# Performance work log

Measured on AMD Instinct MI355X. Metric: run time of the kernel, lower is better.

The kernel has to match this reference:

```python
import jax, jax.numpy as jnp
import numpy as np

B, T, I, H, O = 64, 512, 128, 1024, 128
ALPHA = 0.2


def setup_inputs() -> dict:
    key = jax.random.key(0)
    ks = jax.random.split(key, 7)
    inv_sqrt_h = 1.0 / np.sqrt(H)
    return {
        "x": jax.random.normal(ks[0], (B, T, I), dtype=jnp.float32),
        "wi": jax.random.normal(ks[1], (I, H), dtype=jnp.float32) / np.sqrt(I),
        "wrec": jax.random.normal(ks[2], (H, H), dtype=jnp.float32) * inv_sqrt_h,
        "wout": jax.random.normal(ks[3], (H, O), dtype=jnp.float32) * inv_sqrt_h,
        "b": jax.random.normal(ks[4], (H, 1), dtype=jnp.float32) * 0.1,
        "g": jax.random.normal(ks[5], (H, 1), dtype=jnp.float32) * 0.5 + 1.0,
        "h0": jax.random.normal(ks[6], (H,), dtype=jnp.float32) * 0.1,
    }


def reference(x, wi, wrec, wout, b, g, h0):
    # Leaky tanh RNN: h_{t+1} = h_t + alpha*(-h_t + (g*r_t) @ wrec^T + x_t @ wi)
    #                 r_t = tanh(h_t + b); out_t = (g*r_t) @ wout
    gv = g[:, 0]  # (H,)
    bv = b[:, 0]  # (H,)
    batch = x.shape[0]

    r0 = jnp.tanh(h0 + bv)                     # (H,)
    out0 = (gv * r0) @ wout                    # (O,) broadcast over batch

    h_init = jnp.broadcast_to(h0, (batch, h0.shape[0]))
    r_init = jnp.broadcast_to(r0, (batch, h0.shape[0]))

    # precompute input projection for all steps used in the loop (steps 0..T-2)
    xs = jnp.swapaxes(x[:, :-1, :], 0, 1)      # (T-1, B, I)

    def step(carry, x_t):
        h, r = carry
        h = h + ALPHA * (-h + (gv * r) @ wrec.T + x_t @ wi)
        r = jnp.tanh(h + bv)
        out = (gv * r) @ wout                  # (B, O)
        return (h, r), out

    _, outs = jax.lax.scan(step, (h_init, r_init), xs)   # (T-1, B, O)
    outs = jnp.swapaxes(outs, 0, 1)                      # (B, T-1, O)
    out0b = jnp.broadcast_to(out0, (batch, 1, wout.shape[1]))
    return jnp.concatenate([out0b, outs], axis=1)        # (B, T, O)
```

## Files before the change

kernel.cpp:

```cpp
#include <hip/hip_runtime.h>

#define H 1024
#define I_DIM 128
#define O_DIM 128
#define T_DIM 512
#define ALPHA 0.2f
#define NWG 64
#define GSZ 16
#define PLANE_U64 2048
#define GRP_U64   (3 * PLANE_U64)

typedef short short8 __attribute__((ext_vector_type(8)));
typedef float f32x4 __attribute__((ext_vector_type(4)));
typedef unsigned long long ull_alias __attribute__((may_alias));

__device__ __forceinline__ unsigned short f2b(float f) {
    union { float f; unsigned u; } x; x.f = f;
    unsigned u = x.u;
    return (unsigned short)((u + 0x7FFFu + ((u >> 16) & 1u)) >> 16);
}
__device__ __forceinline__ float tanh_fast(float x) {
    float e = __expf(2.0f * x);
    return 1.0f - 2.0f * __builtin_amdgcn_rcpf(e + 1.0f);
}
__device__ __forceinline__ short8 ld8f(const float* __restrict__ p) {
    const float4 a = *(const float4*)p;
    const float4 b = *(const float4*)(p + 4);
    short8 r;
    r[0]=(short)f2b(a.x); r[1]=(short)f2b(a.y); r[2]=(short)f2b(a.z); r[3]=(short)f2b(a.w);
    r[4]=(short)f2b(b.x); r[5]=(short)f2b(b.y); r[6]=(short)f2b(b.z); r[7]=(short)f2b(b.w);
    return r;
}
__device__ __forceinline__ short8 pack8(float4 a, float4 b) {
    short8 r;
    r[0]=(short)f2b(a.x); r[1]=(short)f2b(a.y); r[2]=(short)f2b(a.z); r[3]=(short)f2b(a.w);
    r[4]=(short)f2b(b.x); r[5]=(short)f2b(b.y); r[6]=(short)f2b(b.z); r[7]=(short)f2b(b.w);
    return r;
}
__device__ __forceinline__ void bar_lgkm() {
    asm volatile("s_waitcnt lgkmcnt(0)\n\ts_barrier" ::: "memory");
}

__global__ __launch_bounds__(256, 1) void rnn_kernel(
    const float* __restrict__ x, const float* __restrict__ wi,
    const float* __restrict__ wrec, const float* __restrict__ wout,
    const float* __restrict__ bb, const float* __restrict__ gg,
    const float* __restrict__ h0p, float* __restrict__ out,
    unsigned long long* __restrict__ aG)
{
    __shared__ unsigned short abuf[32 * 512];
    __shared__ unsigned short aloc[1024];
    __shared__ float opart[4 * 128];

    const int tid  = threadIdx.x;
    const int w    = tid >> 6, lane = tid & 63;
    const int n    = lane & 15, q = lane >> 4;
    const int grp  = blockIdx.x & 3;
    const int ji   = blockIdx.x >> 2;
    const int j0   = ji * 64;
    const int j    = j0 + w * 16 + n;
    const int b0   = grp * 16;

    short8 wfr[32];
#pragma unroll
    for (int kt = 0; kt < 32; ++kt)
        wfr[kt] = ld8f(&wrec[(size_t)j * H + kt * 32 + q * 8]);

    short8 wifr[4];
#pragma unroll
    for (int kt = 0; kt < 4; ++kt) {
        short8 v;
#pragma unroll
        for (int i = 0; i < 8; ++i)
            v[i] = (short)f2b(wi[(size_t)(kt * 32 + q * 8 + i) * H + j]);
        wifr[kt] = v;
    }
    short8 wofr[8];
#pragma unroll
    for (int kk = 0; kk < 8; ++kk) {
        short8 v;
        const int kb = (w * 8 + kk) * 32 + q * 8;
#pragma unroll
        for (int i = 0; i < 8; ++i)
            v[i] = (n < 8) ? (short)f2b(wout[(size_t)(kb + i) * O_DIM + ji * 8 + n]) : (short)0;
        wofr[kk] = v;
    }

    const float gv = gg[j], bv = bb[j], h00 = h0p[j];
    float hreg[4];
#pragma unroll
    for (int r = 0; r < 4; ++r) hreg[r] = h00;

    const int kl    = w * 16 + n;
    const int off_l = (kl >> 5) * 512 + ((kl & 31) >> 3) * 128 + (kl & 7);
    const int s_sl  = ji * 4 + w;

    unsigned long long* const gB0 = aG + grp * GRP_U64;
    unsigned long long* const gB1 = aG + (4 + grp) * GRP_U64;

    const int pubA = (lane >> 5) * PLANE_U64 + s_sl * 32 + (lane & 31);
    const int pubB = 2 * PLANE_U64 + s_sl * 32 + lane;
    const int oA   = lane & 31;

    const int perm  = (lane >> 5) * 32 + (lane & 15) * 2 + ((lane >> 4) & 1);
    const int cb    = w * 512 + perm;

    auto publish = [&](int t) {
        asm volatile("" ::: "memory");
        const unsigned long long tagv = (unsigned long long)(unsigned)t << 48;
        unsigned long long* gb = (t & 1) ? gB1 : gB0;
        {
            const ull_alias* opq = (const ull_alias*)&aloc[w * 256 + (oA & 1) * 128 + (oA >> 1) * 8];
            const unsigned long long lo = opq[0], hi = opq[1];
            const unsigned long long d0 = lo & 0x0000FFFFFFFFFFFFull;
            const unsigned long long d1 = ((lo >> 48) | (hi << 16)) & 0x0000FFFFFFFFFFFFull;
            __hip_atomic_store(gb + pubA, ((lane < 32) ? d0 : d1) | tagv,
                               __ATOMIC_RELAXED, __HIP_MEMORY_SCOPE_AGENT);
        }
        if (lane < 32) {
            const ull_alias* opq = (const ull_alias*)&aloc[w * 256 + (lane & 1) * 128 + (lane >> 1) * 8];
            const unsigned long long hi = opq[1];
            const unsigned long long d2 = ((hi >> 32) & 0xFFFFFFFFull) | tagv;
            __hip_atomic_store(gb + pubB, d2, __ATOMIC_RELAXED, __HIP_MEMORY_SCOPE_AGENT);
        }
    };

    auto poll_issue = [&](const unsigned long long* gb,
                          unsigned long long* v0, unsigned long long* v1,
                          unsigned long long* v2) {
#pragma unroll
        for (int i = 0; i < 8; ++i) {
            v0[i] = __hip_atomic_load(gb + cb + i * 64,
                                      __ATOMIC_RELAXED, __HIP_MEMORY_SCOPE_AGENT);
            v1[i] = __hip_atomic_load(gb + PLANE_U64 + cb + i * 64,
                                      __ATOMIC_RELAXED, __HIP_MEMORY_SCOPE_AGENT);
            v2[i] = __hip_atomic_load(gb + 2 * PLANE_U64 + cb + i * 64,
                                      __ATOMIC_RELAXED, __HIP_MEMORY_SCOPE_AGENT);
        }
    };

    auto poll_check = [&](int tv, const unsigned long long* gb,
                          unsigned long long* v0, unsigned long long* v1,
                          unsigned long long* v2) {
        const unsigned tt = (unsigned)tv;
        for (;;) {
            unsigned bad = 0;
#pragma unroll
            for (int i = 0; i < 8; ++i)
                bad |= ((unsigned)(v0[i] >> 48) ^ tt) | ((unsigned)(v1[i] >> 48) ^ tt)
                     | ((unsigned)(v2[i] >> 48) ^ tt);
            if (__all(bad == 0)) break;
            __builtin_amdgcn_s_sleep(1);
            poll_issue(gb, v0, v1, v2);
        }
        asm volatile("" ::: "memory");
    };

    auto unpack = [&](const unsigned long long* v0, const unsigned long long* v1,
                      const unsigned long long* v2) {
#pragma unroll
        for (int i = 0; i < 8; ++i) {
            const unsigned long long ca = v0[i], cb_ = v1[i], cc = v2[i];
            const unsigned long long w01 = (ca & 0xFFFFFFFFull)
                | (((ca >> 32) & 0xFFFFull) << 32) | ((cb_ & 0xFFFFull) << 48);
            const unsigned long long w23 = ((cb_ >> 16) & 0xFFFFFFFFull) | (cc << 32);
            ull_alias* d = (ull_alias*)((char*)abuf + w * 8192 + (i * 64 + lane) * 16);
            d[0] = w01; d[1] = w23;
        }
    };

    auto do_out = [&](int t) {
        f32x4 oa = {0.f, 0.f, 0.f, 0.f};
#pragma unroll
        for (int kk = 0; kk < 8; ++kk) {
            short8 af = *(const short8*)&abuf[(w * 8 + kk) * 512 + lane * 8];
            oa = __builtin_amdgcn_mfma_f32_16x16x32_bf16(af, wofr[kk], oa, 0, 0, 0);
        }
        if (n < 8) {
#pragma unroll
            for (int r = 0; r < 4; ++r) opart[w * 128 + (4 * q + r) * 8 + n] = oa[r];
        }
        bar_lgkm();
        if (tid < 128) {
            float s = opart[tid] + opart[128 + tid] + opart[256 + tid] + opart[384 + tid];
            const int m = tid >> 3, c = tid & 7;
            out[((size_t)(b0 + m) * T_DIM + t) * O_DIM + ji * 8 + c] = s;
        }
    };

    {
        unsigned short a0 = f2b(gv * tanh_fast(h00 + bv));
#pragma unroll
        for (int r = 0; r < 4; ++r) aloc[off_l + (4 * q + r) * 8] = a0;
        publish(0);
    }

    short8 xfr[4];
#pragma unroll
    for (int kt = 0; kt < 4; ++kt)
        xfr[kt] = ld8f(&x[(size_t)(b0 + n) * T_DIM * I_DIM + kt * 32 + q * 8]);

    float4 xr[8];
    unsigned long long pv0[8], pv1[8], pv2[8];

    for (int t = 1; t < T_DIM; ++t) {
        const unsigned long long* gbp = ((t - 1) & 1) ? gB1 : gB0;

        poll_issue(gbp, pv0, pv1, pv2);

        if (t < T_DIM - 1) {
            const float* xp = &x[((size_t)(b0 + n) * T_DIM + t) * I_DIM];
#pragma unroll
            for (int kt = 0; kt < 4; ++kt) {
                xr[2 * kt]     = *(const float4*)(xp + kt * 32 + q * 8);
                xr[2 * kt + 1] = *(const float4*)(xp + kt * 32 + q * 8 + 4);
            }
        }

        f32x4 acc0 = {0.f,0.f,0.f,0.f}, acc1 = {0.f,0.f,0.f,0.f};
        acc0 = __builtin_amdgcn_mfma_f32_16x16x32_bf16(xfr[0], wifr[0], acc0, 0,0,0);
        acc1 = __builtin_amdgcn_mfma_f32_16x16x32_bf16(xfr[1], wifr[1], acc1, 0,0,0);
        acc0 = __builtin_amdgcn_mfma_f32_16x16x32_bf16(xfr[2], wifr[2], acc0, 0,0,0);
        acc1 = __builtin_amdgcn_mfma_f32_16x16x32_bf16(xfr[3], wifr[3], acc1, 0,0,0);

        bar_lgkm();
        poll_check(t - 1, gbp, pv0, pv1, pv2);
        unpack(pv0, pv1, pv2);
        bar_lgkm();

#pragma unroll
        for (int kt = 0; kt < 32; kt += 2) {
            short8 a0f = *(const short8*)&abuf[kt * 512 + lane * 8];
            short8 a1f = *(const short8*)&abuf[(kt + 1) * 512 + lane * 8];
            acc0 = __builtin_amdgcn_mfma_f32_16x16x32_bf16(a0f, wfr[kt],     acc0, 0,0,0);
            acc1 = __builtin_amdgcn_mfma_f32_16x16x32_bf16(a1f, wfr[kt + 1], acc1, 0,0,0);
        }

#pragma unroll
        for (int r = 0; r < 4; ++r) {
            float z  = acc0[r] + acc1[r];
            float hv = (1.0f - ALPHA) * hreg[r] + ALPHA * z;
            hreg[r] = hv;
            aloc[off_l + (4 * q + r) * 8] = f2b(gv * tanh_fast(hv + bv));
        }
        publish(t);

        if (t < T_DIM - 1) {
#pragma unroll
            for (int kt = 0; kt < 4; ++kt)
                xfr[kt] = pack8(xr[2 * kt], xr[2 * kt + 1]);
        }
        do_out(t - 1);
    }

    poll_issue(gB1, pv0, pv1, pv2);
    bar_lgkm();
    poll_check(T_DIM - 1, gB1, pv0, pv1, pv2);
    unpack(pv0, pv1, pv2);
    bar_lgkm();
    do_out(T_DIM - 1);
}

extern "C" void kernel_launch(void* const* d_in, const int* in_sizes, int n_in,
                              void* d_out, int out_size, void* d_ws, size_t ws_size,
                              hipStream_t stream) {
    const float* x    = (const float*)d_in[0];
    const float* wi   = (const float*)d_in[1];
    const float* wrec = (const float*)d_in[2];
    const float* wout = (const float*)d_in[3];
    const float* bb   = (const float*)d_in[4];
    const float* gg   = (const float*)d_in[5];
    const float* h0   = (const float*)d_in[6];
    float* outp = (float*)d_out;

    unsigned long long* aG = (unsigned long long*)d_ws;

    hipMemsetAsync(d_ws, 0xFF, (size_t)2 * 4 * GRP_U64 * 8, stream);
    hipLaunchKernelGGL(rnn_kernel, dim3(NWG), dim3(256), 0, stream,
                       x, wi, wrec, wout, bb, gg, h0, outp, aG);
}
```

Before: 1.792 ms.

## Repartition RNN across 8 batch groups with 32 hidden columns per wave

Changes the work split from 4 batch groups of 16 rows to 8 groups of 8 rows. Each wave now owns 32 hidden units (two 16-column MFMA tiles), holding twice as many recurrent-weight fragments in registers. The output projection is folded into the recurrent MFMA loop, and one barrier per step is removed by reordering poll, unpack and output writes. The aim is to shrink per-step cross-workgroup exchange and synchronization latency. The costs are that half of each MFMA's 16 rows carry no useful batch data, and the larger register footprint could spill.

```diff
diff --git a/kernel.cpp b/kernel.cpp
--- a/kernel.cpp
+++ b/kernel.cpp
@@ -6,12 +6,14 @@
 #define T_DIM 512
 #define ALPHA 0.2f
 #define NWG 64
-#define GSZ 16
-#define PLANE_U64 2048
-#define GRP_U64   (3 * PLANE_U64)
+#define PLANE_U64 1024
+#define PAR_U64   3072
+#define GRPA_U64  6144
+#define ARENA_U64 49152
 
 typedef short short8 __attribute__((ext_vector_type(8)));
 typedef float f32x4 __attribute__((ext_vector_type(4)));
+typedef unsigned long long u64;
 typedef unsigned long long ull_alias __attribute__((may_alias));
 
 __device__ __forceinline__ unsigned short f2b(float f) {
@@ -46,35 +48,46 @@
     const float* __restrict__ wrec, const float* __restrict__ wout,
     const float* __restrict__ bb, const float* __restrict__ gg,
     const float* __restrict__ h0p, float* __restrict__ out,
-    unsigned long long* __restrict__ aG)
+    u64* __restrict__ aG)
 {
-    __shared__ unsigned short abuf[32 * 512];
+    __shared__ unsigned short abuf[8192];
     __shared__ unsigned short aloc[1024];
-    __shared__ float opart[4 * 128];
+    __shared__ float opart[512];
 
     const int tid  = threadIdx.x;
     const int w    = tid >> 6, lane = tid & 63;
-    const int n    = lane & 15, q = lane >> 4;
-    const int grp  = blockIdx.x & 3;
-    const int ji   = blockIdx.x >> 2;
-    const int j0   = ji * 64;
-    const int j    = j0 + w * 16 + n;
-    const int b0   = grp * 16;
-
-    short8 wfr[32];
-#pragma unroll
-    for (int kt = 0; kt < 32; ++kt)
-        wfr[kt] = ld8f(&wrec[(size_t)j * H + kt * 32 + q * 8]);
-
-    short8 wifr[4];
-#pragma unroll
-    for (int kt = 0; kt < 4; ++kt) {
-        short8 v;
-#pragma unroll
-        for (int i = 0; i < 8; ++i)
-            v[i] = (short)f2b(wi[(size_t)(kt * 32 + q * 8 + i) * H + j]);
-        wifr[kt] = v;
-    }
+    const int q    = lane >> 4;
+    const int n16  = lane & 15;
+    const int mm8  = lane & 7;
+    const int q2   = (lane >> 4) & 1;
+    const int b3   = (lane >> 3) & 1;
+    const int grp  = (int)blockIdx.x & 7;
+    const int ji   = (int)blockIdx.x >> 3;
+    const int b0   = grp * 8;
+    const int jb   = ji * 128 + w * 32;
+    const int s_sl = ji * 4 + w;
+    const int cbg  = w * 256 + lane;
+
+    u64* const gB = aG + (size_t)grp * GRPA_U64;
+
+    short8 wfr[64];
+#pragma unroll
+    for (int nt = 0; nt < 2; ++nt)
+#pragma unroll
+        for (int kt = 0; kt < 32; ++kt)
+            wfr[nt * 32 + kt] = ld8f(&wrec[(size_t)(jb + nt * 16 + n16) * H + kt * 32 + q * 8]);
+
+    short8 wifr[8];
+#pragma unroll
+    for (int nt = 0; nt < 2; ++nt)
+#pragma unroll
+        for (int kt = 0; kt < 4; ++kt) {
+            short8 v;
+#pragma unroll
+            for (int i = 0; i < 8; ++i)
+                v[i] = (short)f2b(wi[(size_t)(kt * 32 + q * 8 + i) * H + jb + nt * 16 + n16]);
+            wifr[nt * 4 + kt] = v;
+        }
     short8 wofr[8];
 #pragma unroll
     for (int kk = 0; kk < 8; ++kk) {
@@ -82,183 +95,196 @@
         const int kb = (w * 8 + kk) * 32 + q * 8;
 #pragma unroll
         for (int i = 0; i < 8; ++i)
-            v[i] = (n < 8) ? (short)f2b(wout[(size_t)(kb + i) * O_DIM + ji * 8 + n]) : (short)0;
+            v[i] = (short)f2b(wout[(size_t)(kb + i) * O_DIM + ji * 16 + n16]);
         wofr[kk] = v;
     }
 
-    const float gv = gg[j], bv = bb[j], h00 = h0p[j];
-    float hreg[4];
-#pragma unroll
-    for (int r = 0; r < 4; ++r) hreg[r] = h00;
-
-    const int kl    = w * 16 + n;
-    const int off_l = (kl >> 5) * 512 + ((kl & 31) >> 3) * 128 + (kl & 7);
-    const int s_sl  = ji * 4 + w;
-
-    unsigned long long* const gB0 = aG + grp * GRP_U64;
-    unsigned long long* const gB1 = aG + (4 + grp) * GRP_U64;
-
-    const int pubA = (lane >> 5) * PLANE_U64 + s_sl * 32 + (lane & 31);
-    const int pubB = 2 * PLANE_U64 + s_sl * 32 + lane;
-    const int oA   = lane & 31;
-
-    const int perm  = (lane >> 5) * 32 + (lane & 15) * 2 + ((lane >> 4) & 1);
-    const int cb    = w * 512 + perm;
-
-    auto publish = [&](int t) {
-        asm volatile("" ::: "memory");
-        const unsigned long long tagv = (unsigned long long)(unsigned)t << 48;
-        unsigned long long* gb = (t & 1) ? gB1 : gB0;
-        {
-            const ull_alias* opq = (const ull_alias*)&aloc[w * 256 + (oA & 1) * 128 + (oA >> 1) * 8];
-            const unsigned long long lo = opq[0], hi = opq[1];
-            const unsigned long long d0 = lo & 0x0000FFFFFFFFFFFFull;
-            const unsigned long long d1 = ((lo >> 48) | (hi << 16)) & 0x0000FFFFFFFFFFFFull;
-            __hip_atomic_store(gb + pubA, ((lane < 32) ? d0 : d1) | tagv,
-                               __ATOMIC_RELAXED, __HIP_MEMORY_SCOPE_AGENT);
-        }
-        if (lane < 32) {
-            const ull_alias* opq = (const ull_alias*)&aloc[w * 256 + (lane & 1) * 128 + (lane >> 1) * 8];
-            const unsigned long long hi = opq[1];
-            const unsigned long long d2 = ((hi >> 32) & 0xFFFFFFFFull) | tagv;
-            __hip_atomic_store(gb + pubB, d2, __ATOMIC_RELAXED, __HIP_MEMORY_SCOPE_AGENT);
+    float gvv[2], bvv[2], hreg[8];
+#pragma unroll
+    for (int nt = 0; nt < 2; ++nt) {
+        const int j = jb + nt * 16 + n16;
+        gvv[nt] = gg[j]; bvv[nt] = bb[j];
+        const float h00 = h0p[j];
+#pragma unroll
+        for (int r = 0; r < 4; ++r) hreg[nt * 4 + r] = h00;
+    }
+
+    short8 xfr[4];
+#pragma unroll
+    for (int kt = 0; kt < 4; ++kt)
+        xfr[kt] = ld8f(&x[(size_t)(b0 + mm8) * T_DIM * I_DIM + kt * 32 + q * 8]);
+
+    if (lane < 32) {
+#pragma unroll
+        for (int nt = 0; nt < 2; ++nt) {
+            const unsigned short a0 = f2b(gvv[nt] * tanh_fast(hreg[nt * 4] + bvv[nt]));
+#pragma unroll
+            for (int r = 0; r < 4; ++r)
+                aloc[w * 256 + ((4 * q2 + r) * 4 + nt * 2 + b3) * 8 + mm8] = a0;
+        }
+    }
+
+    u64 pv0[4], pv1[4], pv2[4];
+
+    auto poll_issue = [&](const u64* gb) {
+#pragma unroll
+        for (int i = 0; i < 4; ++i) {
+            pv0[i] = __hip_atomic_load(gb + cbg + i * 64,
+                                       __ATOMIC_RELAXED, __HIP_MEMORY_SCOPE_AGENT);
+            pv1[i] = __hip_atomic_load(gb + PLANE_U64 + cbg + i * 64,
+                                       __ATOMIC_RELAXED, __HIP_MEMORY_SCOPE_AGENT);
+            pv2[i] = __hip_atomic_load(gb + 2 * PLANE_U64 + cbg + i * 64,
+                                       __ATOMIC_RELAXED, __HIP_MEMORY_SCOPE_AGENT);
         }
     };
-
-    auto poll_issue = [&](const unsigned long long* gb,
-                          unsigned long long* v0, unsigned long long* v1,
-                          unsigned long long* v2) {
-#pragma unroll
-        for (int i = 0; i < 8; ++i) {
-            v0[i] = __hip_atomic_load(gb + cb + i * 64,
-                                      __ATOMIC_RELAXED, __HIP_MEMORY_SCOPE_AGENT);
-            v1[i] = __hip_atomic_load(gb + PLANE_U64 + cb + i * 64,
-                                      __ATOMIC_RELAXED, __HIP_MEMORY_SCOPE_AGENT);
-            v2[i] = __hip_atomic_load(gb + 2 * PLANE_U64 + cb + i * 64,
-                                      __ATOMIC_RELAXED, __HIP_MEMORY_SCOPE_AGENT);
-        }
-    };
-
-    auto poll_check = [&](int tv, const unsigned long long* gb,
-                          unsigned long long* v0, unsigned long long* v1,
-                          unsigned long long* v2) {
+    auto poll_check = [&](int tv, const u64* gb) {
         const unsigned tt = (unsigned)tv;
         for (;;) {
             unsigned bad = 0;
 #pragma unroll
-            for (int i = 0; i < 8; ++i)
-                bad |= ((unsigned)(v0[i] >> 48) ^ tt) | ((unsigned)(v1[i] >> 48) ^ tt)
-                     | ((unsigned)(v2[i] >> 48) ^ tt);
+            for (int i = 0; i < 4; ++i)
+                bad |= ((unsigned)(pv0[i] >> 48) ^ tt) | ((unsigned)(pv1[i] >> 48) ^ tt)
+                     | ((unsigned)(pv2[i] >> 48) ^ tt);
             if (__all(bad == 0)) break;
             __builtin_amdgcn_s_sleep(1);
-            poll_issue(gb, v0, v1, v2);
+            poll_issue(gb);
         }
         asm volatile("" ::: "memory");
     };
-
-    auto unpack = [&](const unsigned long long* v0, const unsigned long long* v1,
-                      const unsigned long long* v2) {
-#pragma unroll
-        for (int i = 0; i < 8; ++i) {
-            const unsigned long long ca = v0[i], cb_ = v1[i], cc = v2[i];
-            const unsigned long long w01 = (ca & 0xFFFFFFFFull)
+    auto unpack = [&]() {
+#pragma unroll
+        for (int i = 0; i < 4; ++i) {
+            const int g  = cbg + i * 64;
+            const int db = ((g >> 5) << 9) | ((g & 3) << 7) | (((g >> 2) & 7) << 4);
+            const u64 ca = pv0[i], cb_ = pv1[i], cc = pv2[i];
+            const u64 w01 = (ca & 0xFFFFFFFFull)
                 | (((ca >> 32) & 0xFFFFull) << 32) | ((cb_ & 0xFFFFull) << 48);
-            const unsigned long long w23 = ((cb_ >> 16) & 0xFFFFFFFFull) | (cc << 32);
-            ull_alias* d = (ull_alias*)((char*)abuf + w * 8192 + (i * 64 + lane) * 16);
+            const u64 w23 = ((cb_ >> 16) & 0xFFFFFFFFull) | (cc << 32);
+            ull_alias* d = (ull_alias*)((char*)abuf + db);
             d[0] = w01; d[1] = w23;
         }
     };
-
-    auto do_out = [&](int t) {
-        f32x4 oa = {0.f, 0.f, 0.f, 0.f};
-#pragma unroll
-        for (int kk = 0; kk < 8; ++kk) {
-            short8 af = *(const short8*)&abuf[(w * 8 + kk) * 512 + lane * 8];
-            oa = __builtin_amdgcn_mfma_f32_16x16x32_bf16(af, wofr[kk], oa, 0, 0, 0);
-        }
-        if (n < 8) {
-#pragma unroll
-            for (int r = 0; r < 4; ++r) opart[w * 128 + (4 * q + r) * 8 + n] = oa[r];
-        }
-        bar_lgkm();
-        if (tid < 128) {
-            float s = opart[tid] + opart[128 + tid] + opart[256 + tid] + opart[384 + tid];
-            const int m = tid >> 3, c = tid & 7;
-            out[((size_t)(b0 + m) * T_DIM + t) * O_DIM + ji * 8 + c] = s;
+    auto publish = [&](int t) {
+        asm volatile("s_waitcnt lgkmcnt(0)" ::: "memory");
+        const u64 tagv = (u64)(unsigned)t << 48;
+        u64* gb = gB + ((t & 1) ? PAR_U64 : 0);
+        const ull_alias* opq = (const ull_alias*)&aloc[w * 256 + (lane & 31) * 8];
+        const u64 lo = opq[0], hi = opq[1];
+        const u64 d01 = (lane < 32) ? (lo & 0x0000FFFFFFFFFFFFull)
+                                    : (((lo >> 48) | (hi << 16)) & 0x0000FFFFFFFFFFFFull);
+        u64* pA = gb + (lane >> 5) * PLANE_U64 + s_sl * 32 + (lane & 31);
+        __hip_atomic_store(pA, d01 | tagv, __ATOMIC_RELAXED, __HIP_MEMORY_SCOPE_AGENT);
+        if (lane < 32) {
+            const u64 d2 = ((hi >> 32) & 0xFFFFFFFFull) | tagv;
+            u64* pB = gb + 2 * PLANE_U64 + s_sl * 32 + lane;
+            __hip_atomic_store(pB, d2, __ATOMIC_RELAXED, __HIP_MEMORY_SCOPE_AGENT);
         }
     };
 
-    {
-        unsigned short a0 = f2b(gv * tanh_fast(h00 + bv));
-#pragma unroll
-        for (int r = 0; r < 4; ++r) aloc[off_l + (4 * q + r) * 8] = a0;
-        publish(0);
-    }
-
-    short8 xfr[4];
-#pragma unroll
-    for (int kt = 0; kt < 4; ++kt)
-        xfr[kt] = ld8f(&x[(size_t)(b0 + n) * T_DIM * I_DIM + kt * 32 + q * 8]);
+    const int fro = q * 64 + mm8 * 8;
+    publish(0);
 
     float4 xr[8];
-    unsigned long long pv0[8], pv1[8], pv2[8];
-
     for (int t = 1; t < T_DIM; ++t) {
-        const unsigned long long* gbp = ((t - 1) & 1) ? gB1 : gB0;
-
-        poll_issue(gbp, pv0, pv1, pv2);
+        const u64* gbp = gB + (((t - 1) & 1) ? PAR_U64 : 0);
+        poll_issue(gbp);
 
         if (t < T_DIM - 1) {
-            const float* xp = &x[((size_t)(b0 + n) * T_DIM + t) * I_DIM];
+            const float* xp = &x[((size_t)(b0 + mm8) * T_DIM + t) * I_DIM];
 #pragma unroll
             for (int kt = 0; kt < 4; ++kt) {
                 xr[2 * kt]     = *(const float4*)(xp + kt * 32 + q * 8);
                 xr[2 * kt + 1] = *(const float4*)(xp + kt * 32 + q * 8 + 4);
             }
         }
-
-        f32x4 acc0 = {0.f,0.f,0.f,0.f}, acc1 = {0.f,0.f,0.f,0.f};
-        acc0 = __builtin_amdgcn_mfma_f32_16x16x32_bf16(xfr[0], wifr[0], acc0, 0,0,0);
-        acc1 = __builtin_amdgcn_mfma_f32_16x16x32_bf16(xfr[1], wifr[1], acc1, 0,0,0);
-        acc0 = __builtin_amdgcn_mfma_f32_16x16x32_bf16(xfr[2], wifr[2], acc0, 0,0,0);
-        acc1 = __builtin_amdgcn_mfma_f32_16x16x32_bf16(xfr[3], wifr[3], acc1, 0,0,0);
-
+        f32x4 xacc0 = {0.f,0.f,0.f,0.f}, xacc1 = {0.f,0.f,0.f,0.f};
+#pragma unroll
+        for (int kt = 0; kt < 4; ++kt) {
+            xacc0 = __builtin_amdgcn_mfma_f32_16x16x32_bf16(xfr[kt], wifr[kt],     xacc0, 0,0,0);
+            xacc1 = __builtin_amdgcn_mfma_f32_16x16x32_bf16(xfr[kt], wifr[4 + kt], xacc1, 0,0,0);
+        }
+
+        poll_check(t - 1, gbp);
+        unpack();
         bar_lgkm();
-        poll_check(t - 1, gbp, pv0, pv1, pv2);
-        unpack(pv0, pv1, pv2);
-        bar_lgkm();
-
+
+        f32x4 acc00 = {0.f,0.f,0.f,0.f}, acc01 = {0.f,0.f,0.f,0.f};
+        f32x4 acc10 = {0.f,0.f,0.f,0.f}, acc11 = {0.f,0.f,0.f,0.f};
+        f32x4 oa    = {0.f,0.f,0.f,0.f};
 #pragma unroll
         for (int kt = 0; kt < 32; kt += 2) {
-            short8 a0f = *(const short8*)&abuf[kt * 512 + lane * 8];
-            short8 a1f = *(const short8*)&abuf[(kt + 1) * 512 + lane * 8];
-            acc0 = __builtin_amdgcn_mfma_f32_16x16x32_bf16(a0f, wfr[kt],     acc0, 0,0,0);
-            acc1 = __builtin_amdgcn_mfma_f32_16x16x32_bf16(a1f, wfr[kt + 1], acc1, 0,0,0);
-        }
-
-#pragma unroll
-        for (int r = 0; r < 4; ++r) {
-            float z  = acc0[r] + acc1[r];
-            float hv = (1.0f - ALPHA) * hreg[r] + ALPHA * z;
-            hreg[r] = hv;
-            aloc[off_l + (4 * q + r) * 8] = f2b(gv * tanh_fast(hv + bv));
+            short8 af0 = *(const short8*)&abuf[kt * 256 + fro];
+            short8 af1 = *(const short8*)&abuf[(kt + 1) * 256 + fro];
+            acc00 = __builtin_amdgcn_mfma_f32_16x16x32_bf16(af0, wfr[kt],          acc00, 0,0,0);
+            acc01 = __builtin_amdgcn_mfma_f32_16x16x32_bf16(af1, wfr[kt + 1],      acc01, 0,0,0);
+            acc10 = __builtin_amdgcn_mfma_f32_16x16x32_bf16(af0, wfr[32 + kt],     acc10, 0,0,0);
+            acc11 = __builtin_amdgcn_mfma_f32_16x16x32_bf16(af1, wfr[32 + kt + 1], acc11, 0,0,0);
+            if ((kt >> 3) == w) {
+                oa = __builtin_amdgcn_mfma_f32_16x16x32_bf16(af0, wofr[kt & 7],       oa, 0,0,0);
+                oa = __builtin_amdgcn_mfma_f32_16x16x32_bf16(af1, wofr[(kt + 1) & 7], oa, 0,0,0);
+            }
+        }
+
+#pragma unroll
+        for (int nt = 0; nt < 2; ++nt) {
+            const f32x4 a0 = nt ? acc10 : acc00;
+            const f32x4 a1 = nt ? acc11 : acc01;
+            const f32x4 xa = nt ? xacc1 : xacc0;
+#pragma unroll
+            for (int r = 0; r < 4; ++r) {
+                const float z  = xa[r] + a0[r] + a1[r];
+                const float hv = (1.0f - ALPHA) * hreg[nt * 4 + r] + ALPHA * z;
+                hreg[nt * 4 + r] = hv;
+                if (lane < 32) {
+                    const unsigned short av = f2b(gvv[nt] * tanh_fast(hv + bvv[nt]));
+                    aloc[w * 256 + ((4 * q2 + r) * 4 + nt * 2 + b3) * 8 + mm8] = av;
+                }
+            }
         }
         publish(t);
 
+        if (lane < 32) {
+#pragma unroll
+            for (int r = 0; r < 4; ++r)
+                opart[w * 128 + (4 * q2 + r) * 16 + n16] = oa[r];
+        }
         if (t < T_DIM - 1) {
 #pragma unroll
             for (int kt = 0; kt < 4; ++kt)
                 xfr[kt] = pack8(xr[2 * kt], xr[2 * kt + 1]);
         }
-        do_out(t - 1);
-    }
-
-    poll_issue(gB1, pv0, pv1, pv2);
-    bar_lgkm();
-    poll_check(T_DIM - 1, gB1, pv0, pv1, pv2);
-    unpack(pv0, pv1, pv2);
-    bar_lgkm();
-    do_out(T_DIM - 1);
+        bar_lgkm();
+        if (tid < 128) {
+            const float s = opart[tid] + opart[128 + tid] + opart[256 + tid] + opart[384 + tid];
+            const int m = tid >> 4, c = tid & 15;
+            out[((size_t)(b0 + m) * T_DIM + (t - 1)) * O_DIM + ji * 16 + c] = s;
+        }
+    }
+
+    {
+        const u64* gbe = gB + PAR_U64;
+        poll_issue(gbe);
+        poll_check(T_DIM - 1, gbe);
+        unpack();
+        bar_lgkm();
+        f32x4 oa = {0.f,0.f,0.f,0.f};
+#pragma unroll
+        for (int kk = 0; kk < 8; ++kk) {
+            short8 af = *(const short8*)&abuf[(w * 8 + kk) * 256 + fro];
+            oa = __builtin_amdgcn_mfma_f32_16x16x32_bf16(af, wofr[kk], oa, 0, 0, 0);
+        }
+        if (lane < 32) {
+#pragma unroll
+            for (int r = 0; r < 4; ++r)
+                opart[w * 128 + (4 * q2 + r) * 16 + n16] = oa[r];
+        }
+        bar_lgkm();
+        if (tid < 128) {
+            const float s = opart[tid] + opart[128 + tid] + opart[256 + tid] + opart[384 + tid];
+            const int m = tid >> 4, c = tid & 15;
+            out[((size_t)(b0 + m) * T_DIM + (T_DIM - 1)) * O_DIM + ji * 16 + c] = s;
+        }
+    }
 }
 
 extern "C" void kernel_launch(void* const* d_in, const int* in_sizes, int n_in,
@@ -273,9 +299,9 @@
     const float* h0   = (const float*)d_in[6];
     float* outp = (float*)d_out;
 
-    unsigned long long* aG = (unsigned long long*)d_ws;
-
-    hipMemsetAsync(d_ws, 0xFF, (size_t)2 * 4 * GRP_U64 * 8, stream);
+    u64* aG = (u64*)d_ws;
+
+    hipMemsetAsync(d_ws, 0xFF, (size_t)ARENA_U64 * sizeof(u64), stream);
     hipLaunchKernelGGL(rnn_kernel, dim3(NWG), dim3(256), 0, stream,
                        x, wi, wrec, wout, bb, gg, h0, outp, aG);
 }
```

Result: slower. 2.143 ms (+19.6%).

## Double-buffer activation LDS and defer output projection into poll-wait window

Applied to the files above, without the earlier changes.

The shared activation buffer is split into two halves so the output projection for step t-2 can run from the previous buffer while the block waits for step t-1's published activations. The output GEMM moves off the critical path after publish and into the spin-wait slot, and one barrier before polling is removed. The cost is double the LDS for abuf and added hazard reasoning around the opart barrier inside do_out.

```diff
diff --git a/kernel.cpp b/kernel.cpp
--- a/kernel.cpp
+++ b/kernel.cpp
@@ -6,12 +6,12 @@
 #define T_DIM 512
 #define ALPHA 0.2f
 #define NWG 64
-#define GSZ 16
 #define PLANE_U64 2048
 #define GRP_U64   (3 * PLANE_U64)
 
 typedef short short8 __attribute__((ext_vector_type(8)));
 typedef float f32x4 __attribute__((ext_vector_type(4)));
+typedef unsigned long long u64;
 typedef unsigned long long ull_alias __attribute__((may_alias));
 
 __device__ __forceinline__ unsigned short f2b(float f) {
@@ -46,9 +46,9 @@
     const float* __restrict__ wrec, const float* __restrict__ wout,
     const float* __restrict__ bb, const float* __restrict__ gg,
     const float* __restrict__ h0p, float* __restrict__ out,
-    unsigned long long* __restrict__ aG)
+    u64* __restrict__ aG)
 {
-    __shared__ unsigned short abuf[32 * 512];
+    __shared__ unsigned short abuf[2][16384];
     __shared__ unsigned short aloc[1024];
     __shared__ float opart[4 * 128];
 
@@ -95,8 +95,8 @@
     const int off_l = (kl >> 5) * 512 + ((kl & 31) >> 3) * 128 + (kl & 7);
     const int s_sl  = ji * 4 + w;
 
-    unsigned long long* const gB0 = aG + grp * GRP_U64;
-    unsigned long long* const gB1 = aG + (4 + grp) * GRP_U64;
+    u64* const gB0 = aG + grp * GRP_U64;
+    u64* const gB1 = aG + (4 + grp) * GRP_U64;
 
     const int pubA = (lane >> 5) * PLANE_U64 + s_sl * 32 + (lane & 31);
     const int pubB = 2 * PLANE_U64 + s_sl * 32 + lane;
@@ -106,74 +106,69 @@
     const int cb    = w * 512 + perm;
 
     auto publish = [&](int t) {
-        asm volatile("" ::: "memory");
-        const unsigned long long tagv = (unsigned long long)(unsigned)t << 48;
-        unsigned long long* gb = (t & 1) ? gB1 : gB0;
+        asm volatile("s_waitcnt lgkmcnt(0)" ::: "memory");
+        const u64 tagv = (u64)(unsigned)t << 48;
+        u64* gb = (t & 1) ? gB1 : gB0;
         {
             const ull_alias* opq = (const ull_alias*)&aloc[w * 256 + (oA & 1) * 128 + (oA >> 1) * 8];
-            const unsigned long long lo = opq[0], hi = opq[1];
-            const unsigned long long d0 = lo & 0x0000FFFFFFFFFFFFull;
-            const unsigned long long d1 = ((lo >> 48) | (hi << 16)) & 0x0000FFFFFFFFFFFFull;
+            const u64 lo = opq[0], hi = opq[1];
+            const u64 d0 = lo & 0x0000FFFFFFFFFFFFull;
+            const u64 d1 = ((lo >> 48) | (hi << 16)) & 0x0000FFFFFFFFFFFFull;
             __hip_atomic_store(gb + pubA, ((lane < 32) ? d0 : d1) | tagv,
                                __ATOMIC_RELAXED, __HIP_MEMORY_SCOPE_AGENT);
         }
         if (lane < 32) {
             const ull_alias* opq = (const ull_alias*)&aloc[w * 256 + (lane & 1) * 128 + (lane >> 1) * 8];
-            const unsigned long long hi = opq[1];
-            const unsigned long long d2 = ((hi >> 32) & 0xFFFFFFFFull) | tagv;
+            const u64 hi = opq[1];
+            const u64 d2 = ((hi >> 32) & 0xFFFFFFFFull) | tagv;
             __hip_atomic_store(gb + pubB, d2, __ATOMIC_RELAXED, __HIP_MEMORY_SCOPE_AGENT);
         }
     };
 
-    auto poll_issue = [&](const unsigned long long* gb,
-                          unsigned long long* v0, unsigned long long* v1,
-                          unsigned long long* v2) {
+    u64 pv0[8], pv1[8], pv2[8];
+
+    auto poll_issue = [&](const u64* gb) {
 #pragma unroll
         for (int i = 0; i < 8; ++i) {
-            v0[i] = __hip_atomic_load(gb + cb + i * 64,
-                                      __ATOMIC_RELAXED, __HIP_MEMORY_SCOPE_AGENT);
-            v1[i] = __hip_atomic_load(gb + PLANE_U64 + cb + i * 64,
-                                      __ATOMIC_RELAXED, __HIP_MEMORY_SCOPE_AGENT);
-            v2[i] = __hip_atomic_load(gb + 2 * PLANE_U64 + cb + i * 64,
-                                      __ATOMIC_RELAXED, __HIP_MEMORY_SCOPE_AGENT);
-        }
-    };
-
-    auto poll_check = [&](int tv, const unsigned long long* gb,
-                          unsigned long long* v0, unsigned long long* v1,
-                          unsigned long long* v2) {
+            pv0[i] = __hip_atomic_load(gb + cb + i * 64,
+                                       __ATOMIC_RELAXED, __HIP_MEMORY_SCOPE_AGENT);
+            pv1[i] = __hip_atomic_load(gb + PLANE_U64 + cb + i * 64,
+                                       __ATOMIC_RELAXED, __HIP_MEMORY_SCOPE_AGENT);
+            pv2[i] = __hip_atomic_load(gb + 2 * PLANE_U64 + cb + i * 64,
+                                       __ATOMIC_RELAXED, __HIP_MEMORY_SCOPE_AGENT);
+        }
+    };
+    auto poll_check = [&](int tv, const u64* gb) {
         const unsigned tt = (unsigned)tv;
         for (;;) {
             unsigned bad = 0;
 #pragma unroll
             for (int i = 0; i < 8; ++i)
-                bad |= ((unsigned)(v0[i] >> 48) ^ tt) | ((unsigned)(v1[i] >> 48) ^ tt)
-                     | ((unsigned)(v2[i] >> 48) ^ tt);
+                bad |= ((unsigned)(pv0[i] >> 48) ^ tt) | ((unsigned)(pv1[i] >> 48) ^ tt)
+                     | ((unsigned)(pv2[i] >> 48) ^ tt);
             if (__all(bad == 0)) break;
             __builtin_amdgcn_s_sleep(1);
-            poll_issue(gb, v0, v1, v2);
+            poll_issue(gb);
         }
         asm volatile("" ::: "memory");
     };
-
-    auto unpack = [&](const unsigned long long* v0, const unsigned long long* v1,
-                      const unsigned long long* v2) {
+    auto unpack = [&](unsigned short* ab) {
 #pragma unroll
         for (int i = 0; i < 8; ++i) {
-            const unsigned long long ca = v0[i], cb_ = v1[i], cc = v2[i];
-            const unsigned long long w01 = (ca & 0xFFFFFFFFull)
+            const u64 ca = pv0[i], cb_ = pv1[i], cc = pv2[i];
+            const u64 w01 = (ca & 0xFFFFFFFFull)
                 | (((ca >> 32) & 0xFFFFull) << 32) | ((cb_ & 0xFFFFull) << 48);
-            const unsigned long long w23 = ((cb_ >> 16) & 0xFFFFFFFFull) | (cc << 32);
-            ull_alias* d = (ull_alias*)((char*)abuf + w * 8192 + (i * 64 + lane) * 16);
+            const u64 w23 = ((cb_ >> 16) & 0xFFFFFFFFull) | (cc << 32);
+            ull_alias* d = (ull_alias*)((char*)ab + w * 8192 + (i * 64 + lane) * 16);
             d[0] = w01; d[1] = w23;
         }
     };
 
-    auto do_out = [&](int t) {
+    auto do_out = [&](int t, const unsigned short* ab) {
         f32x4 oa = {0.f, 0.f, 0.f, 0.f};
 #pragma unroll
         for (int kk = 0; kk < 8; ++kk) {
-            short8 af = *(const short8*)&abuf[(w * 8 + kk) * 512 + lane * 8];
+            short8 af = *(const short8*)&ab[(w * 8 + kk) * 512 + lane * 8];
             oa = __builtin_amdgcn_mfma_f32_16x16x32_bf16(af, wofr[kk], oa, 0, 0, 0);
         }
         if (n < 8) {
@@ -201,12 +196,13 @@
         xfr[kt] = ld8f(&x[(size_t)(b0 + n) * T_DIM * I_DIM + kt * 32 + q * 8]);
 
     float4 xr[8];
-    unsigned long long pv0[8], pv1[8], pv2[8];
 
     for (int t = 1; t < T_DIM; ++t) {
-        const unsigned long long* gbp = ((t - 1) & 1) ? gB1 : gB0;
-
-        poll_issue(gbp, pv0, pv1, pv2);
+        const u64* gbp = ((t - 1) & 1) ? gB1 : gB0;
+        unsigned short* cur  = abuf[(t - 1) & 1];
+        unsigned short* prev = abuf[t & 1];
+
+        poll_issue(gbp);
 
         if (t < T_DIM - 1) {
             const float* xp = &x[((size_t)(b0 + n) * T_DIM + t) * I_DIM];
@@ -223,15 +219,16 @@
         acc0 = __builtin_amdgcn_mfma_f32_16x16x32_bf16(xfr[2], wifr[2], acc0, 0,0,0);
         acc1 = __builtin_amdgcn_mfma_f32_16x16x32_bf16(xfr[3], wifr[3], acc1, 0,0,0);
 
-        bar_lgkm();
-        poll_check(t - 1, gbp, pv0, pv1, pv2);
-        unpack(pv0, pv1, pv2);
+        if (t >= 2) do_out(t - 2, prev);
+
+        poll_check(t - 1, gbp);
+        unpack(cur);
         bar_lgkm();
 
 #pragma unroll
         for (int kt = 0; kt < 32; kt += 2) {
-            short8 a0f = *(const short8*)&abuf[kt * 512 + lane * 8];
-            short8 a1f = *(const short8*)&abuf[(kt + 1) * 512 + lane * 8];
+            short8 a0f = *(const short8*)&cur[kt * 512 + lane * 8];
+            short8 a1f = *(const short8*)&cur[(kt + 1) * 512 + lane * 8];
             acc0 = __builtin_amdgcn_mfma_f32_16x16x32_bf16(a0f, wfr[kt],     acc0, 0,0,0);
             acc1 = __builtin_amdgcn_mfma_f32_16x16x32_bf16(a1f, wfr[kt + 1], acc1, 0,0,0);
         }
@@ -250,15 +247,17 @@
             for (int kt = 0; kt < 4; ++kt)
                 xfr[kt] = pack8(xr[2 * kt], xr[2 * kt + 1]);
         }
-        do_out(t - 1);
-    }
-
-    poll_issue(gB1, pv0, pv1, pv2);
-    bar_lgkm();
-    poll_check(T_DIM - 1, gB1, pv0, pv1, pv2);
-    unpack(pv0, pv1, pv2);
-    bar_lgkm();
-    do_out(T_DIM - 1);
+    }
+
+    {
+        poll_issue(gB1);
+        poll_check(T_DIM - 1, gB1);
+        unpack(abuf[1]);
+        bar_lgkm();
+        do_out(T_DIM - 2, abuf[0]);
+        bar_lgkm();
+        do_out(T_DIM - 1, abuf[1]);
+    }
 }
 
 extern "C" void kernel_launch(void* const* d_in, const int* in_sizes, int n_in,
@@ -273,7 +272,7 @@
     const float* h0   = (const float*)d_in[6];
     float* outp = (float*)d_out;
 
-    unsigned long long* aG = (unsigned long long*)d_ws;
+    u64* aG = (u64*)d_ws;
 
     hipMemsetAsync(d_ws, 0xFF, (size_t)2 * 4 * GRP_U64 * 8, stream);
     hipLaunchKernelGGL(rnn_kernel, dim3(NWG), dim3(256), 0, stream,
```

Measured after the change: 1.855 ms. 1.04x slower.
